# Kernel tuning notes

Measured on AMD Instinct MI355X. Metric: run time of the kernel, lower is better.

## Reference

```python
import jax, jax.numpy as jnp
import numpy as np
from jax import lax

B, V, N = 32, 3, 128          # batch, views, worm points
H, W = 512, 512               # image_size
DECAY_FACTOR = 10.0           # MAX_DECAY_FACTOR buffer value
OOB = 1e-05                   # oob_grad_val
MAX_STEPS = 10
LR, ALPHA, EPS = 0.2, 0.99, 1e-08  # torch.optim.RMSprop defaults (lr=0.2)

_b = jnp.arange(B)[:, None, None]   # (B,1,1)
_c = jnp.arange(V)[None, :, None]   # (1,3,1)


def _get_yx(p):
    # round -> long -> clamp to [0, H-1]; col 1 is y (row), col 0 is x (col)
    pi = jnp.clip(jnp.round(p).astype(jnp.int32), 0, H - 1)
    return pi[..., 1], pi[..., 0]  # each (B,3,N)


def _points_to_masks(p):
    y, x = _get_yx(p)
    return jnp.zeros((B, V, H, W), jnp.float32).at[_b, _c, y, x].set(1.0)


def _gradient_surface(masks_diff):
    grad0 = -masks_diff  # (B,3,H,W)
    grads = [grad0]
    g = grad0
    while g.shape[-1] > 1:
        gp = jnp.pad(g, ((0, 0), (0, 0), (1, 1), (1, 1)), constant_values=OOB)
        g = lax.reduce_window(gp, 0.0, lax.add, (1, 1, 3, 3), (1, 1, 2, 2), 'VALID') / 9.0
        grads.append(g)
    gs = jnp.zeros_like(grad0)
    for g in grads:
        # F.interpolate bilinear align_corners=False == jax.image.resize 'linear'
        gs = gs + jax.image.resize(g, grad0.shape, 'linear')
    ga = gs / len(grads)
    gapx = jnp.pad(ga, ((0, 0), (0, 0), (1, 1), (0, 0)), mode='edge')
    gx = (gapx[:, :, :-2] - gapx[:, :, 2:]) * 0.5   # central diff along H
    gapy = jnp.pad(ga, ((0, 0), (0, 0), (0, 0), (1, 1)), mode='edge')
    gy = (gapy[..., :-2] - gapy[..., 2:]) * 0.5     # central diff along W
    return jnp.stack([gx, gy])  # (2,B,3,H,W)


def setup_inputs() -> dict:
    key = jax.random.key(0)
    k1, k2 = jax.random.split(key)
    points_2d = jax.random.uniform(k1, (B, V, N, 2), jnp.float32) * (H - 1)
    masks_target = jax.random.uniform(k2, (B, V, H, W), jnp.float32)
    return {'points_2d': points_2d, 'masks_target': masks_target}


def reference(points_2d, masks_target):
    decay = jnp.exp(-jnp.arange(N, dtype=jnp.float32) / N * DECAY_FACTOR)  # (N,)
    masks_out = _points_to_masks(points_2d)
    masks_diff = masks_target - 0.01 * masks_out
    J = _gradient_surface(masks_diff)  # (2,B,3,H,W)
    p0 = lax.stop_gradient(points_2d)  # matches .clone().detach()

    def body(carry, _):
        p, sq, done = carry
        y, x = _get_yx(p)
        pl = (1.0 - masks_target[_b, _c, y, x]) * decay  # (B,3,N)
        cont = pl.max() > 0.1
        active = jnp.logical_and(jnp.logical_not(done), cont)
        gxp = J[0][_b, _c, y, x]
        gyp = J[1][_b, _c, y, x]
        g = -jnp.stack([gyp, gxp], axis=-1) * pl[..., None]  # (B,3,N,2)
        # RMSprop step
        sq_n = ALPHA * sq + (1.0 - ALPHA) * g * g
        p_n = p - LR * g / (jnp.sqrt(sq_n) + EPS)
        p = jnp.where(active, p_n, p)
        sq = jnp.where(active, sq_n, sq)
        done = jnp.logical_or(done, jnp.logical_not(cont))
        return (p, sq, done), None

    (p_opt, _, _), _ = lax.scan(body, (p0, jnp.zeros_like(p0), jnp.array(False)), None, length=MAX_STEPS)
    masks_opt = _points_to_masks(p_opt)
    return masks_out, masks_opt, p_opt
```

## Files before the change

### kernel.cpp

```cpp
#include <hip/hip_runtime.h>

#define IMGS 96
#define HW   262144
#define NPTS 12288
#define OOBV 1e-5f

static constexpr size_t PYR_OFF   = 0;
static constexpr size_t P_OFF     = 8388576;
static constexpr size_t SQ_OFF    = 8413152;
static constexpr size_t PLMAX_OFF = 8437728;
static constexpr size_t CNT_OFF   = 8437739;
static constexpr size_t LIST_OFF  = 8437740;

__device__ __forceinline__ int clampi(int v, int lo, int hi) {
    v = v < lo ? lo : v;
    return v > hi ? hi : v;
}

__global__ void k_scatter(const float* __restrict__ pts, float* __restrict__ mo,
                          int* __restrict__ cnt, int* __restrict__ plist) {
    int i = blockIdx.x * blockDim.x + threadIdx.x;
    if (i >= NPTS) return;
    float px = pts[2*i], py = pts[2*i+1];
    int xi = clampi((int)rintf(px), 0, 511);
    int yi = clampi((int)rintf(py), 0, 511);
    int gp = (i >> 7) * HW + yi * 512 + xi;
    float old = atomicExch(&mo[gp], 1.0f);
    if (old == 0.0f) {
        int k = atomicAdd(cnt, 1);
        plist[k] = gp;
    }
}

__global__ void k_lvl1(const float* __restrict__ mt, float* __restrict__ out) {
    int t = blockIdx.x * blockDim.x + threadIdx.x;
    if (t >= IMGS * 65536) return;
    int j = t & 255, i = (t >> 8) & 255, img = t >> 16;
    const float* m = mt + (size_t)img * HW;
    float s = 0.0f;
    #pragma unroll
    for (int dy = -1; dy <= 1; ++dy) {
        int y = 2*i + dy;
        #pragma unroll
        for (int dx = -1; dx <= 1; ++dx) {
            int x = 2*j + dx;
            s += (y >= 0 && y < 512 && x >= 0 && x < 512) ? -m[y*512 + x] : OOBV;
        }
    }
    out[t] = s / 9.0f;
}

__global__ void k_corr1(const int* __restrict__ cnt, const int* __restrict__ plist,
                        float* __restrict__ lvl1) {
    int k = blockIdx.x * blockDim.x + threadIdx.x;
    if (k >= *cnt) return;
    int gp = plist[k];
    int img = gp >> 18;
    int r = gp & (HW - 1);
    int y = r >> 9, x = r & 511;
    float* L = lvl1 + (size_t)img * 65536;
    const float c = 0.01f / 9.0f;
    int ilo = y >> 1, ihi = ((y + 1) >> 1) > 255 ? 255 : ((y + 1) >> 1);
    int jlo = x >> 1, jhi = ((x + 1) >> 1) > 255 ? 255 : ((x + 1) >> 1);
    for (int i = ilo; i <= ihi; ++i)
        for (int j = jlo; j <= jhi; ++j)
            atomicAdd(&L[i*256 + j], c);
}

__global__ void k_lvl(const float* __restrict__ in, float* __restrict__ out,
                      int sin, int sout) {
    int t = blockIdx.x * blockDim.x + threadIdx.x;
    int ss = sout * sout;
    if (t >= IMGS * ss) return;
    int img = t / ss;
    int r = t - img * ss;
    int i = r / sout;
    int j = r - i * sout;
    const float* m = in + (size_t)img * sin * sin;
    float s = 0.0f;
    for (int dy = -1; dy <= 1; ++dy) {
        int y = 2*i + dy;
        for (int dx = -1; dx <= 1; ++dx) {
            int x = 2*j + dx;
            s += (y >= 0 && y < sin && x >= 0 && x < sin) ? m[y*sin + x] : OOBV;
        }
    }
    out[t] = s / 9.0f;
}

__global__ __launch_bounds__(256) void k_ga(const float* __restrict__ mt,
                                            const float* __restrict__ pyr,
                                            float* __restrict__ ga) {
    __shared__ float vrow[520];
    int img = blockIdx.x >> 9;
    int h = blockIdx.x & 511;
    float hf = (float)h;

    for (int e = threadIdx.x; e < 520; e += 256) {
        int l = 0, rem = e;
        while (true) {
            int len = (256 >> l) + 1;
            if (rem < len) break;
            rem -= len; ++l;
        }
        int s = 256 >> l;
        int x = rem < s ? rem : s - 1;
        float scale = (float)s * (1.0f / 512.0f);
        float fy = (hf + 0.5f) * scale - 0.5f;
        fy = fminf(fmaxf(fy, 0.0f), (float)(s - 1));
        float fyf = floorf(fy);
        int y0 = (int)fyf;
        float ty = fy - fyf;
        int yb = (y0 + 1 < s) ? y0 + 1 : s - 1;
        const float* Lp = pyr + (8388608 - (8388608 >> (2*l))) + (size_t)img * s * s;
        float a = Lp[y0*s + x], b = Lp[yb*s + x];
        vrow[e] = (1.0f - ty) * a + ty * b;
    }
    __syncthreads();

    #pragma unroll
    for (int rep = 0; rep < 2; ++rep) {
        int w = threadIdx.x + rep * 256;
        int idx = img * HW + h * 512 + w;
        float wf = (float)w;
        float acc = -mt[idx];
        #pragma unroll
        for (int l = 0; l < 9; ++l) {
            const int s = 256 >> l;
            const float scale = (float)s * (1.0f / 512.0f);
            float fx = (wf + 0.5f) * scale - 0.5f;
            fx = fminf(fmaxf(fx, 0.0f), (float)(s - 1));
            float fxf = floorf(fx);
            int x0 = (int)fxf;
            float tx = fx - fxf;
            const int vo = 512 - (512 >> l) + l;
            float a = vrow[vo + x0], b = vrow[vo + x0 + 1];
            acc += (1.0f - tx) * a + tx * b;
        }
        ga[idx] = acc / 10.0f;
    }
}

__global__ void k_corrga(const int* __restrict__ cnt, const int* __restrict__ plist,
                         float* __restrict__ ga) {
    int k = blockIdx.x * blockDim.x + threadIdx.x;
    if (k >= *cnt) return;
    ga[plist[k]] += 0.001f;
}

__global__ void k_init(const float* __restrict__ pts, const float* __restrict__ mt,
                       float* __restrict__ p, float* __restrict__ sq,
                       float* __restrict__ plmax) {
    int i = blockIdx.x * blockDim.x + threadIdx.x;
    if (i >= NPTS) return;
    float px = pts[2*i], py = pts[2*i+1];
    p[2*i] = px; p[2*i+1] = py;
    sq[2*i] = 0.0f; sq[2*i+1] = 0.0f;
    int xi = clampi((int)rintf(px), 0, 511);
    int yi = clampi((int)rintf(py), 0, 511);
    int img = i >> 7, n = i & 127;
    float d = expf(-(float)n * 0.078125f);
    float pl = (1.0f - mt[(size_t)img * HW + yi*512 + xi]) * d;
    atomicMax((int*)plmax, __float_as_int(pl));
}

__global__ void k_step(const float* __restrict__ mt, const float* __restrict__ ga,
                       float* __restrict__ p, float* __restrict__ sq,
                       float* __restrict__ plmax, int t) {
    int i = blockIdx.x * blockDim.x + threadIdx.x;
    if (i >= NPTS) return;
    float plm = plmax[t];
    if (!(plm > 0.1f)) {
        if (i == 0) plmax[t+1] = plm;
        return;
    }
    float px = p[2*i], py = p[2*i+1];
    int xi = clampi((int)rintf(px), 0, 511);
    int yi = clampi((int)rintf(py), 0, 511);
    int img = i >> 7, n = i & 127;
    const float* M = mt + (size_t)img * HW;
    const float* G = ga + (size_t)img * HW;
    float d = expf(-(float)n * 0.078125f);
    float pl = (1.0f - M[yi*512 + xi]) * d;
    float gxp = (G[clampi(yi-1,0,511)*512 + xi] - G[clampi(yi+1,0,511)*512 + xi]) * 0.5f;
    float gyp = (G[yi*512 + clampi(xi-1,0,511)] - G[yi*512 + clampi(xi+1,0,511)]) * 0.5f;
    float g0 = -gyp * pl;
    float g1 = -gxp * pl;
    float s0 = 0.99f * sq[2*i]   + 0.01f * g0 * g0;
    float s1 = 0.99f * sq[2*i+1] + 0.01f * g1 * g1;
    float p0 = px - 0.2f * g0 / (sqrtf(s0) + 1e-8f);
    float p1 = py - 0.2f * g1 / (sqrtf(s1) + 1e-8f);
    p[2*i] = p0; p[2*i+1] = p1;
    sq[2*i] = s0; sq[2*i+1] = s1;
    int xi2 = clampi((int)rintf(p0), 0, 511);
    int yi2 = clampi((int)rintf(p1), 0, 511);
    float pl2 = (1.0f - M[yi2*512 + xi2]) * d;
    atomicMax((int*)(plmax + t + 1), __float_as_int(pl2));
}

__global__ void k_final(const float* __restrict__ p, float* __restrict__ mopt,
                        float* __restrict__ pout) {
    int i = blockIdx.x * blockDim.x + threadIdx.x;
    if (i >= NPTS) return;
    float px = p[2*i], py = p[2*i+1];
    pout[2*i] = px; pout[2*i+1] = py;
    int xi = clampi((int)rintf(px), 0, 511);
    int yi = clampi((int)rintf(py), 0, 511);
    mopt[(i >> 7) * HW + yi*512 + xi] = 1.0f;
}

extern "C" void kernel_launch(void* const* d_in, const int* in_sizes, int n_in,
                              void* d_out, int out_size, void* d_ws, size_t ws_size,
                              hipStream_t stream) {
    const float* pts = (const float*)d_in[0];
    const float* mt  = (const float*)d_in[1];
    if (in_sizes[0] != NPTS * 2) { const float* tmp = pts; pts = mt; mt = tmp; }

    float* out  = (float*)d_out;
    float* mo   = out;
    float* ga   = out + (size_t)IMGS * HW;
    float* pout = out + 2 * (size_t)IMGS * HW;

    float* ws    = (float*)d_ws;
    float* pyr   = ws + PYR_OFF;
    float* p     = ws + P_OFF;
    float* sq    = ws + SQ_OFF;
    float* plmax = ws + PLMAX_OFF;
    int*   cnt   = (int*)(ws + CNT_OFF);
    int*   plist = (int*)(ws + LIST_OFF);

    hipMemsetAsync(mo, 0, (size_t)IMGS * HW * sizeof(float), stream);
    hipMemsetAsync(plmax, 0, 12 * sizeof(float), stream);

    k_scatter<<<NPTS/256, 256, 0, stream>>>(pts, mo, cnt, plist);
    k_lvl1<<<IMGS*65536/256, 256, 0, stream>>>(mt, pyr);
    k_corr1<<<NPTS/256, 256, 0, stream>>>(cnt, plist, pyr);

    int offs[10];
    offs[1] = 0;
    for (int l = 2; l <= 9; ++l) {
        int sprev = 512 >> (l - 1);
        offs[l] = offs[l-1] + IMGS * sprev * sprev;
    }
    for (int l = 2; l <= 9; ++l) {
        int sin = 512 >> (l - 1), sout = 512 >> l;
        int tot = IMGS * sout * sout;
        k_lvl<<<(tot + 255)/256, 256, 0, stream>>>(pyr + offs[l-1], pyr + offs[l], sin, sout);
    }

    k_ga<<<IMGS*512, 256, 0, stream>>>(mt, pyr, ga);
    k_corrga<<<NPTS/256, 256, 0, stream>>>(cnt, plist, ga);
    k_init<<<NPTS/256, 256, 0, stream>>>(pts, mt, p, sq, plmax);
    for (int t = 0; t < 10; ++t)
        k_step<<<NPTS/256, 256, 0, stream>>>(mt, ga, p, sq, plmax, t);

    hipMemsetAsync(ga, 0, (size_t)IMGS * HW * sizeof(float), stream);
    k_final<<<NPTS/256, 256, 0, stream>>>(p, ga, pout);
}
```

Baseline: 482.1 us.

## Fuse small pyramid levels into one shared-memory kernel and merge init into scatter

Levels 3 through 9 of the pyramid are now built by a single per-image kernel that keeps the intermediate levels in shared memory, replacing seven separate tiny launches. Level 2 gets a specialised kernel with constant sizes. The init work is merged into the scatter kernel. The ga surface moves to workspace, so one memset of the whole output replaces the two separate memsets and the output region no longer has to be re-zeroed before the final scatter. The aim is to cut launch overhead and extra memset traffic, at the cost of a small-grid tail kernel with only 96 blocks.

Result: no change. 482.8 us (+0.1%).

```diff
diff --git a/kernel.cpp b/kernel.cpp
--- a/kernel.cpp
+++ b/kernel.cpp
@@ -11,25 +11,34 @@
 static constexpr size_t PLMAX_OFF = 8437728;
 static constexpr size_t CNT_OFF   = 8437739;
 static constexpr size_t LIST_OFF  = 8437740;
+static constexpr size_t GA_OFF    = 8450560;
 
 __device__ __forceinline__ int clampi(int v, int lo, int hi) {
     v = v < lo ? lo : v;
     return v > hi ? hi : v;
 }
 
-__global__ void k_scatter(const float* __restrict__ pts, float* __restrict__ mo,
-                          int* __restrict__ cnt, int* __restrict__ plist) {
+__global__ void k_scatter_init(const float* __restrict__ pts, const float* __restrict__ mt,
+                               float* __restrict__ mo, int* __restrict__ cnt,
+                               int* __restrict__ plist, float* __restrict__ p,
+                               float* __restrict__ sq, float* __restrict__ plmax) {
     int i = blockIdx.x * blockDim.x + threadIdx.x;
     if (i >= NPTS) return;
     float px = pts[2*i], py = pts[2*i+1];
     int xi = clampi((int)rintf(px), 0, 511);
     int yi = clampi((int)rintf(py), 0, 511);
-    int gp = (i >> 7) * HW + yi * 512 + xi;
+    int img = i >> 7, n = i & 127;
+    int gp = img * HW + yi * 512 + xi;
     float old = atomicExch(&mo[gp], 1.0f);
     if (old == 0.0f) {
         int k = atomicAdd(cnt, 1);
         plist[k] = gp;
     }
+    p[2*i] = px; p[2*i+1] = py;
+    sq[2*i] = 0.0f; sq[2*i+1] = 0.0f;
+    float d = expf(-(float)n * 0.078125f);
+    float pl = (1.0f - mt[(size_t)img * HW + yi*512 + xi]) * d;
+    atomicMax((int*)plmax, __float_as_int(pl));
 }
 
 __global__ void k_lvl1(const float* __restrict__ mt, float* __restrict__ out) {
@@ -67,25 +76,68 @@
             atomicAdd(&L[i*256 + j], c);
 }
 
-__global__ void k_lvl(const float* __restrict__ in, float* __restrict__ out,
-                      int sin, int sout) {
+__global__ void k_lvl2(const float* __restrict__ in, float* __restrict__ out) {
     int t = blockIdx.x * blockDim.x + threadIdx.x;
-    int ss = sout * sout;
-    if (t >= IMGS * ss) return;
-    int img = t / ss;
-    int r = t - img * ss;
-    int i = r / sout;
-    int j = r - i * sout;
-    const float* m = in + (size_t)img * sin * sin;
+    if (t >= IMGS * 16384) return;
+    int j = t & 127, i = (t >> 7) & 127, img = t >> 14;
+    const float* m = in + (size_t)img * 65536;
     float s = 0.0f;
+    #pragma unroll
     for (int dy = -1; dy <= 1; ++dy) {
         int y = 2*i + dy;
+        #pragma unroll
         for (int dx = -1; dx <= 1; ++dx) {
             int x = 2*j + dx;
-            s += (y >= 0 && y < sin && x >= 0 && x < sin) ? m[y*sin + x] : OOBV;
+            s += (y >= 0 && y < 256 && x >= 0 && x < 256) ? m[y*256 + x] : OOBV;
         }
     }
     out[t] = s / 9.0f;
+}
+
+__global__ __launch_bounds__(256) void k_pyrtail(float* __restrict__ pyr) {
+    __shared__ float buf[5461];
+    int img = blockIdx.x;
+    const float* L2 = pyr + 6291456 + (size_t)img * 16384;
+    for (int t = threadIdx.x; t < 4096; t += 256) {
+        int i = t >> 6, j = t & 63;
+        float s = 0.0f;
+        #pragma unroll
+        for (int dy = -1; dy <= 1; ++dy) {
+            int y = 2*i + dy;
+            #pragma unroll
+            for (int dx = -1; dx <= 1; ++dx) {
+                int x = 2*j + dx;
+                s += (y >= 0 && y < 128 && x >= 0 && x < 128) ? L2[y*128 + x] : OOBV;
+            }
+        }
+        float v = s / 9.0f;
+        buf[t] = v;
+        pyr[7864320 + (size_t)img * 4096 + t] = v;
+    }
+    __syncthreads();
+    int inOff = 0, sin = 64;
+    size_t goff = 8257536;
+    while (sin > 1) {
+        int sout = sin >> 1;
+        int outOff = inOff + sin * sin;
+        for (int t = threadIdx.x; t < sout * sout; t += 256) {
+            int i = t / sout, j = t - i * sout;
+            float s = 0.0f;
+            for (int dy = -1; dy <= 1; ++dy) {
+                int y = 2*i + dy;
+                for (int dx = -1; dx <= 1; ++dx) {
+                    int x = 2*j + dx;
+                    s += (y >= 0 && y < sin && x >= 0 && x < sin) ? buf[inOff + y*sin + x] : OOBV;
+                }
+            }
+            float v = s / 9.0f;
+            buf[outOff + t] = v;
+            pyr[goff + (size_t)img * sout * sout + t] = v;
+        }
+        __syncthreads();
+        inOff = outOff; sin = sout;
+        goff += (size_t)96 * sout * sout;
+    }
 }
 
 __global__ __launch_bounds__(256) void k_ga(const float* __restrict__ mt,
@@ -146,22 +198,6 @@
     int k = blockIdx.x * blockDim.x + threadIdx.x;
     if (k >= *cnt) return;
     ga[plist[k]] += 0.001f;
-}
-
-__global__ void k_init(const float* __restrict__ pts, const float* __restrict__ mt,
-                       float* __restrict__ p, float* __restrict__ sq,
-                       float* __restrict__ plmax) {
-    int i = blockIdx.x * blockDim.x + threadIdx.x;
-    if (i >= NPTS) return;
-    float px = pts[2*i], py = pts[2*i+1];
-    p[2*i] = px; p[2*i+1] = py;
-    sq[2*i] = 0.0f; sq[2*i+1] = 0.0f;
-    int xi = clampi((int)rintf(px), 0, 511);
-    int yi = clampi((int)rintf(py), 0, 511);
-    int img = i >> 7, n = i & 127;
-    float d = expf(-(float)n * 0.078125f);
-    float pl = (1.0f - mt[(size_t)img * HW + yi*512 + xi]) * d;
-    atomicMax((int*)plmax, __float_as_int(pl));
 }
 
 __global__ void k_step(const float* __restrict__ mt, const float* __restrict__ ga,
@@ -218,7 +254,7 @@
 
     float* out  = (float*)d_out;
     float* mo   = out;
-    float* ga   = out + (size_t)IMGS * HW;
+    float* mopt = out + (size_t)IMGS * HW;
     float* pout = out + 2 * (size_t)IMGS * HW;
 
     float* ws    = (float*)d_ws;
@@ -228,32 +264,19 @@
     float* plmax = ws + PLMAX_OFF;
     int*   cnt   = (int*)(ws + CNT_OFF);
     int*   plist = (int*)(ws + LIST_OFF);
-
-    hipMemsetAsync(mo, 0, (size_t)IMGS * HW * sizeof(float), stream);
+    float* ga    = ws + GA_OFF;
+
+    hipMemsetAsync(out, 0, (size_t)out_size * sizeof(float), stream);
     hipMemsetAsync(plmax, 0, 12 * sizeof(float), stream);
 
-    k_scatter<<<NPTS/256, 256, 0, stream>>>(pts, mo, cnt, plist);
+    k_scatter_init<<<NPTS/256, 256, 0, stream>>>(pts, mt, mo, cnt, plist, p, sq, plmax);
     k_lvl1<<<IMGS*65536/256, 256, 0, stream>>>(mt, pyr);
     k_corr1<<<NPTS/256, 256, 0, stream>>>(cnt, plist, pyr);
-
-    int offs[10];
-    offs[1] = 0;
-    for (int l = 2; l <= 9; ++l) {
-        int sprev = 512 >> (l - 1);
-        offs[l] = offs[l-1] + IMGS * sprev * sprev;
-    }
-    for (int l = 2; l <= 9; ++l) {
-        int sin = 512 >> (l - 1), sout = 512 >> l;
-        int tot = IMGS * sout * sout;
-        k_lvl<<<(tot + 255)/256, 256, 0, stream>>>(pyr + offs[l-1], pyr + offs[l], sin, sout);
-    }
-
+    k_lvl2<<<IMGS*16384/256, 256, 0, stream>>>(pyr, pyr + 6291456);
+    k_pyrtail<<<IMGS, 256, 0, stream>>>(pyr);
     k_ga<<<IMGS*512, 256, 0, stream>>>(mt, pyr, ga);
     k_corrga<<<NPTS/256, 256, 0, stream>>>(cnt, plist, ga);
-    k_init<<<NPTS/256, 256, 0, stream>>>(pts, mt, p, sq, plmax);
     for (int t = 0; t < 10; ++t)
         k_step<<<NPTS/256, 256, 0, stream>>>(mt, ga, p, sq, plmax, t);
-
-    hipMemsetAsync(ga, 0, (size_t)IMGS * HW * sizeof(float), stream);
-    k_final<<<NPTS/256, 256, 0, stream>>>(p, ga, pout);
-}
+    k_final<<<NPTS/256, 256, 0, stream>>>(p, mopt, pout);
+}
```
